# Kernel optimization log

Hardware: AMD Instinct MI355X
Metric: run time of the kernel (lower is better)

Reference implementation:

```python
import jax, jax.numpy as jnp
import numpy as np

N, IN_SIZE, HEADS, OUT_SIZE = 2048, 256, 4, 32


def setup_inputs() -> dict:
    key = jax.random.key(0)
    k_adj, k_h, k_w, k_a = jax.random.split(key, 4)
    # adj strictly positive so the masked softmax over the heads axis has no
    # all-(-inf) slices (the repo code softmaxes over dim=1 == heads, so any
    # zero adjacency entry would yield NaN). Mask op is still exercised.
    adj = jax.random.uniform(k_adj, (N, N), dtype=jnp.float32)
    h = jax.random.normal(k_h, (N, IN_SIZE), dtype=jnp.float32)
    W = jax.random.normal(k_w, (HEADS * OUT_SIZE, IN_SIZE), dtype=jnp.float32) * 0.08
    attn_a = jax.random.normal(k_a, (1, HEADS, 2 * OUT_SIZE), dtype=jnp.float32) * 0.1
    return {"adj": adj, "h": h, "W": W, "attn_a": attn_a}


def reference(adj, h, W, attn_a):
    # fc (no bias): [N, in] @ [in, heads*out] -> [N, heads, out]
    n = h.shape[0]
    heads = attn_a.shape[1]
    out = attn_a.shape[2] // 2
    feat = (h @ W.T).reshape(n, heads, out)
    # el = cat([f_src, f_dst]); er = cat([f_dst, f_src]); src == dst here so
    # both dot-products with attn are identical -> e = leaky_relu(2 * s).
    el = jnp.concatenate([feat, feat], axis=2)          # [N, heads, 2*out]
    s = jnp.einsum('nhd,hd->nh', el, attn_a[0])          # bmm(el, attn^T) squeezed
    e = jax.nn.leaky_relu(s + s, negative_slope=0.01)    # [N, heads]
    # attention[i, h, j] = e[i, h] where adj[i, j] > 0 else -inf
    att = jnp.where(adj[:, None, :] > 0, e[:, :, None], -jnp.inf)  # [N, heads, N]
    # NOTE: softmax over the HEADS axis (dim=1), faithful to the source.
    att = jax.nn.softmax(att, axis=1)
    # bmm(attention.transpose(1,2), feat): [N, N, heads] @ [N, heads, out]
    h_prime = jnp.einsum('nhj,nho->njo', att, feat)      # [N, N, out]
    return h_prime
```

## Files before the change

### kernel.cpp

```cpp
#include <hip/hip_runtime.h>
#include <math.h>

#define GN 2048
#define GIN 256
#define GHEADS 4
#define GOUT 32
#define GNH (GHEADS * GOUT)

typedef float f32x4 __attribute__((ext_vector_type(4)));

__global__ __launch_bounds__(256) void
DenseGATLayer_90108413870812_kernel(const float* __restrict__ adj,
                                    const float* __restrict__ h,
                                    const float* __restrict__ W,
                                    const float* __restrict__ attn_a,
                                    f32x4* __restrict__ out)
{
    const int n   = blockIdx.x;
    const int tid = threadIdx.x;

    __shared__ float sh_adj[GN];
    __shared__ float sh_h[GIN];
    __shared__ float sh_tmp[GNH];
    __shared__ float sh_s[GHEADS];
    __shared__ float sh_g[GOUT];

    const f32x4* arow4 = reinterpret_cast<const f32x4*>(adj + (size_t)n * GN);
    const f32x4 a0 = arow4[tid];
    const f32x4 a1 = arow4[tid + 256];
    float2 h2 = {0.f, 0.f};
    if (tid < 128) {
        const float2* hr = reinterpret_cast<const float2*>(h + (size_t)n * GIN);
        h2 = hr[tid];
    }
    reinterpret_cast<f32x4*>(sh_adj)[tid]       = a0;
    reinterpret_cast<f32x4*>(sh_adj)[tid + 256] = a1;
    if (tid < 128)
        reinterpret_cast<float2*>(sh_h)[tid] = h2;
    __syncthreads();

    float feat = 0.f;
    const int head = tid >> 5;
    if (tid < GNH) {
        const int o = tid & 31;

        const f32x4* Wr = reinterpret_cast<const f32x4*>(W + (size_t)tid * GIN);
        const f32x4* hv = reinterpret_cast<const f32x4*>(sh_h);
        float s0 = 0.f, s1 = 0.f, s2 = 0.f, s3 = 0.f;
        #pragma unroll 8
        for (int k4 = 0; k4 < GIN / 4; ++k4) {
            f32x4 w4 = Wr[k4];
            f32x4 h4 = hv[k4];
            s0 = fmaf(h4.x, w4.x, s0);
            s1 = fmaf(h4.y, w4.y, s1);
            s2 = fmaf(h4.z, w4.z, s2);
            s3 = fmaf(h4.w, w4.w, s3);
        }
        feat = (s0 + s1) + (s2 + s3);

        const float aco = attn_a[head * (2 * GOUT) + o] +
                          attn_a[head * (2 * GOUT) + GOUT + o];
        float p = feat * aco;
        #pragma unroll
        for (int m = 16; m >= 1; m >>= 1)
            p += __shfl_xor(p, m, 64);
        if (o == 0) sh_s[head] = p;
    }
    __syncthreads();

    if (tid < GNH) {
        float e[GHEADS];
        float mx = -INFINITY;
        #pragma unroll
        for (int i = 0; i < GHEADS; ++i) {
            const float s2 = 2.f * sh_s[i];
            e[i] = (s2 > 0.f) ? s2 : 0.01f * s2;
            mx = fmaxf(mx, e[i]);
        }
        float denom = 0.f;
        #pragma unroll
        for (int i = 0; i < GHEADS; ++i) {
            e[i] = expf(e[i] - mx);
            denom += e[i];
        }
        sh_tmp[tid] = (e[head] / denom) * feat;
    }
    __syncthreads();

    if (tid < GOUT) {
        sh_g[tid] = sh_tmp[tid] + sh_tmp[tid + 32] +
                    sh_tmp[tid + 64] + sh_tmp[tid + 96];
    }
    __syncthreads();

    const int q = tid & 7;
    const f32x4 gq = reinterpret_cast<const f32x4*>(sh_g)[q];
    const float nanv = __builtin_nanf("");
    const f32x4 nan4 = { nanv, nanv, nanv, nanv };

    f32x4* __restrict__ orow = out + (size_t)n * (GN * (GOUT / 4));
    const int jbase = tid >> 3;

    #pragma unroll 8
    for (int iter = 0; iter < (GN * (GOUT / 4)) / 256; ++iter) {
        const float av = sh_adj[jbase + iter * 32];
        const f32x4 v = (av > 0.f) ? gq : nan4;
        orow[tid + iter * 256] = v;
    }
}

extern "C" void kernel_launch(void* const* d_in, const int* in_sizes, int n_in,
                              void* d_out, int out_size, void* d_ws, size_t ws_size,
                              hipStream_t stream) {
    const float* adj    = (const float*)d_in[0];
    const float* h      = (const float*)d_in[1];
    const float* W      = (const float*)d_in[2];
    const float* attn_a = (const float*)d_in[3];
    f32x4* out = (f32x4*)d_out;

    DenseGATLayer_90108413870812_kernel<<<GN, 256, 0, stream>>>(adj, h, W, attn_a, out);
}
```

Before: 545.6 us.

## Split GAT into batched feature-vector kernel and pure streaming store kernel

Moves the per-row projection, head-softmax and head reduction into a separate kernel that processes 8 rows per block, reusing each W row across 4 rows per thread instead of rereading W for every node. The second kernel only loads the adjacency row and the precomputed 32-float vector, then streams the masked output. This removes the redundant W traffic and the serial compute phase ahead of the output writes, at the cost of an extra kernel launch and a workspace round trip.

```diff
diff --git a/kernel.cpp b/kernel.cpp
--- a/kernel.cpp
+++ b/kernel.cpp
@@ -9,92 +9,108 @@
 
 typedef float f32x4 __attribute__((ext_vector_type(4)));
 
-__global__ __launch_bounds__(256) void
-DenseGATLayer_90108413870812_kernel(const float* __restrict__ adj,
-                                    const float* __restrict__ h,
-                                    const float* __restrict__ W,
-                                    const float* __restrict__ attn_a,
-                                    f32x4* __restrict__ out)
+
+__global__ __launch_bounds__(256) void gat_gvec(
+    const float* __restrict__ h, const float* __restrict__ W,
+    const float* __restrict__ attn_a, float* __restrict__ g)
+{
+    const int n0  = blockIdx.x * 8;
+    const int tid = threadIdx.x;
+
+    __shared__ f32x4 sh_h4[8 * 64];
+    __shared__ float sh_s[8][GHEADS];
+    __shared__ float sh_wf[8][GNH];
+
+    const f32x4* h4 = reinterpret_cast<const f32x4*>(h) + (size_t)n0 * 64;
+    sh_h4[tid]       = h4[tid];
+    sh_h4[tid + 256] = h4[tid + 256];
+    __syncthreads();
+
+    const int c    = tid & 127;
+    const int rg   = tid >> 7;
+    const int head = c >> 5;
+    const int o    = c & 31;
+
+    const f32x4* Wr = reinterpret_cast<const f32x4*>(W) + (size_t)c * 64;
+    f32x4 ac0 = {0,0,0,0}, ac1 = {0,0,0,0}, ac2 = {0,0,0,0}, ac3 = {0,0,0,0};
+    const f32x4* hb = &sh_h4[rg * 4 * 64];
+    #pragma unroll 4
+    for (int k4 = 0; k4 < 64; ++k4) {
+        const f32x4 w4 = Wr[k4];
+        ac0 += w4 * hb[k4];
+        ac1 += w4 * hb[64 + k4];
+        ac2 += w4 * hb[128 + k4];
+        ac3 += w4 * hb[192 + k4];
+    }
+    float feat0 = (ac0.x + ac0.y) + (ac0.z + ac0.w);
+    float feat1 = (ac1.x + ac1.y) + (ac1.z + ac1.w);
+    float feat2 = (ac2.x + ac2.y) + (ac2.z + ac2.w);
+    float feat3 = (ac3.x + ac3.y) + (ac3.z + ac3.w);
+
+    const float aco = attn_a[head * (2 * GOUT) + o] +
+                      attn_a[head * (2 * GOUT) + GOUT + o];
+    float p0 = feat0 * aco, p1 = feat1 * aco, p2 = feat2 * aco, p3 = feat3 * aco;
+    #pragma unroll
+    for (int m = 16; m >= 1; m >>= 1) {
+        p0 += __shfl_xor(p0, m, 64);
+        p1 += __shfl_xor(p1, m, 64);
+        p2 += __shfl_xor(p2, m, 64);
+        p3 += __shfl_xor(p3, m, 64);
+    }
+    if (o == 0) {
+        sh_s[rg * 4 + 0][head] = p0;
+        sh_s[rg * 4 + 1][head] = p1;
+        sh_s[rg * 4 + 2][head] = p2;
+        sh_s[rg * 4 + 3][head] = p3;
+    }
+    __syncthreads();
+
+    const float ft[4] = {feat0, feat1, feat2, feat3};
+    #pragma unroll
+    for (int r = 0; r < 4; ++r) {
+        const int row = rg * 4 + r;
+        float e[GHEADS];
+        float mx = -INFINITY;
+        #pragma unroll
+        for (int i = 0; i < GHEADS; ++i) {
+            const float s2 = 2.f * sh_s[row][i];
+            e[i] = (s2 > 0.f) ? s2 : 0.01f * s2;
+            mx = fmaxf(mx, e[i]);
+        }
+        float denom = 0.f;
+        #pragma unroll
+        for (int i = 0; i < GHEADS; ++i) { e[i] = expf(e[i] - mx); denom += e[i]; }
+        sh_wf[row][c] = (e[head] / denom) * ft[r];
+    }
+    __syncthreads();
+
+    {
+        const int row = tid >> 5;
+        const int oo  = tid & 31;
+        g[(size_t)(n0 + row) * GOUT + oo] =
+            sh_wf[row][oo] + sh_wf[row][32 + oo] +
+            sh_wf[row][64 + oo] + sh_wf[row][96 + oo];
+    }
+}
+
+__global__ __launch_bounds__(256) void gat_store(
+    const float* __restrict__ adj, const float* __restrict__ g,
+    f32x4* __restrict__ out)
 {
     const int n   = blockIdx.x;
     const int tid = threadIdx.x;
 
     __shared__ float sh_adj[GN];
-    __shared__ float sh_h[GIN];
-    __shared__ float sh_tmp[GNH];
-    __shared__ float sh_s[GHEADS];
-    __shared__ float sh_g[GOUT];
 
     const f32x4* arow4 = reinterpret_cast<const f32x4*>(adj + (size_t)n * GN);
     const f32x4 a0 = arow4[tid];
     const f32x4 a1 = arow4[tid + 256];
-    float2 h2 = {0.f, 0.f};
-    if (tid < 128) {
-        const float2* hr = reinterpret_cast<const float2*>(h + (size_t)n * GIN);
-        h2 = hr[tid];
-    }
+    const int q = tid & 7;
+    const f32x4 gq = reinterpret_cast<const f32x4*>(g)[n * 8 + q];
     reinterpret_cast<f32x4*>(sh_adj)[tid]       = a0;
     reinterpret_cast<f32x4*>(sh_adj)[tid + 256] = a1;
-    if (tid < 128)
-        reinterpret_cast<float2*>(sh_h)[tid] = h2;
     __syncthreads();
 
-    float feat = 0.f;
-    const int head = tid >> 5;
-    if (tid < GNH) {
-        const int o = tid & 31;
-
-        const f32x4* Wr = reinterpret_cast<const f32x4*>(W + (size_t)tid * GIN);
-        const f32x4* hv = reinterpret_cast<const f32x4*>(sh_h);
-        float s0 = 0.f, s1 = 0.f, s2 = 0.f, s3 = 0.f;
-        #pragma unroll 8
-        for (int k4 = 0; k4 < GIN / 4; ++k4) {
-            f32x4 w4 = Wr[k4];
-            f32x4 h4 = hv[k4];
-            s0 = fmaf(h4.x, w4.x, s0);
-            s1 = fmaf(h4.y, w4.y, s1);
-            s2 = fmaf(h4.z, w4.z, s2);
-            s3 = fmaf(h4.w, w4.w, s3);
-        }
-        feat = (s0 + s1) + (s2 + s3);
-
-        const float aco = attn_a[head * (2 * GOUT) + o] +
-                          attn_a[head * (2 * GOUT) + GOUT + o];
-        float p = feat * aco;
-        #pragma unroll
-        for (int m = 16; m >= 1; m >>= 1)
-            p += __shfl_xor(p, m, 64);
-        if (o == 0) sh_s[head] = p;
-    }
-    __syncthreads();
-
-    if (tid < GNH) {
-        float e[GHEADS];
-        float mx = -INFINITY;
-        #pragma unroll
-        for (int i = 0; i < GHEADS; ++i) {
-            const float s2 = 2.f * sh_s[i];
-            e[i] = (s2 > 0.f) ? s2 : 0.01f * s2;
-            mx = fmaxf(mx, e[i]);
-        }
-        float denom = 0.f;
-        #pragma unroll
-        for (int i = 0; i < GHEADS; ++i) {
-            e[i] = expf(e[i] - mx);
-            denom += e[i];
-        }
-        sh_tmp[tid] = (e[head] / denom) * feat;
-    }
-    __syncthreads();
-
-    if (tid < GOUT) {
-        sh_g[tid] = sh_tmp[tid] + sh_tmp[tid + 32] +
-                    sh_tmp[tid + 64] + sh_tmp[tid + 96];
-    }
-    __syncthreads();
-
-    const int q = tid & 7;
-    const f32x4 gq = reinterpret_cast<const f32x4*>(sh_g)[q];
     const float nanv = __builtin_nanf("");
     const f32x4 nan4 = { nanv, nanv, nanv, nanv };
 
@@ -117,6 +133,8 @@
     const float* W      = (const float*)d_in[2];
     const float* attn_a = (const float*)d_in[3];
     f32x4* out = (f32x4*)d_out;
+    float* g   = (float*)d_ws;
 
-    DenseGATLayer_90108413870812_kernel<<<GN, 256, 0, stream>>>(adj, h, W, attn_a, out);
+    gat_gvec <<<GN / 8, 256, 0, stream>>>(h, W, attn_a, g);
+    gat_store<<<GN,     256, 0, stream>>>(adj, g, out);
 }
```

After: 539.8 us. About the same (-1.1%).
